# Kernel optimization log

Hardware: AMD Instinct MI355X
Metric: run time of the kernel (lower is better)

Reference implementation:

```python
import jax, jax.numpy as jnp
import numpy as np

PH = PW = 7      # aligned output bins (output_size=(aligned_width, aligned_height)=(7,7))
SR = 2           # fixed bilinear sampling ratio per bin (approximates torchvision adaptive ratio)
NUM_LEVELS = 4


def _sample_offsets(n_bins):
    # offsets (in units of bin size) of SR samples per bin: py + (iy+0.5)/SR
    k = jnp.arange(n_bins * SR, dtype=jnp.float32)
    return (k // SR) + ((k % SR) + 0.5) / SR  # [n_bins*SR]


def _bilinear_gather(feat, ys, xs):
    # feat [C,H,W]; ys [N,I]; xs [N,J] -> [N,C,I,J]  (torchvision bilinear_interpolate semantics)
    C, H, W = feat.shape
    vy = (ys >= -1.0) & (ys <= H)
    vx = (xs >= -1.0) & (xs <= W)
    y = jnp.clip(ys, 0.0, H - 1.0)
    x = jnp.clip(xs, 0.0, W - 1.0)
    y0 = jnp.floor(y)
    x0 = jnp.floor(x)
    ly = y - y0
    lx = x - x0
    y0i = y0.astype(jnp.int32)
    x0i = x0.astype(jnp.int32)
    y1i = jnp.minimum(y0i + 1, H - 1)
    x1i = jnp.minimum(x0i + 1, W - 1)

    def g(yi, xi):
        return feat[:, yi[:, :, None], xi[:, None, :]]  # [C,N,I,J]

    w00 = (1.0 - ly)[:, :, None] * (1.0 - lx)[:, None, :]
    w01 = (1.0 - ly)[:, :, None] * lx[:, None, :]
    w10 = ly[:, :, None] * (1.0 - lx)[:, None, :]
    w11 = ly[:, :, None] * lx[:, None, :]
    val = (w00 * g(y0i, x0i) + w01 * g(y0i, x1i)
           + w10 * g(y1i, x0i) + w11 * g(y1i, x1i))  # [C,N,I,J]
    mask = vy[:, :, None] & vx[:, None, :]            # [N,I,J]
    return jnp.where(mask[None], val, 0.0).transpose(1, 0, 2, 3)


def _roi_align_level(feat, boxes):
    # feat [C,H,W], boxes [N,4] xyxy in this level's coords -> [N,C,PH,PW]
    x1, y1, x2, y2 = boxes[:, 0], boxes[:, 1], boxes[:, 2], boxes[:, 3]
    rw = jnp.maximum(x2 - x1, 1.0)
    rh = jnp.maximum(y2 - y1, 1.0)
    bw = rw / PW
    bh = rh / PH
    ys = y1[:, None] + _sample_offsets(PH)[None, :] * bh[:, None]  # [N, PH*SR]
    xs = x1[:, None] + _sample_offsets(PW)[None, :] * bw[:, None]  # [N, PW*SR]
    v = _bilinear_gather(feat, ys, xs)                             # [N,C,PH*SR,PW*SR]
    N, C = v.shape[0], v.shape[1]
    return v.reshape(N, C, PH, SR, PW, SR).mean(axis=(3, 5))       # avg over samples per bin


def setup_inputs() -> dict:
    key = jax.random.key(0)
    kf0, kf1, kf2, kf3, kxy, klev = jax.random.split(key, 6)
    B, C, H0, N = 2, 256, 160, 512
    feats = {}
    for name, k, hw in (("feat0", kf0, 160), ("feat1", kf1, 80), ("feat2", kf2, 40), ("feat3", kf3, 20)):
        feats[name] = jax.random.normal(k, (B, C, hw, hw), dtype=jnp.float32)
    # boxes xyxy in base (pre-scale) coords, in [0, ~19.5]
    xy = jnp.sort(jax.random.uniform(kxy, (B, N, 2, 2), dtype=jnp.float32) * 19.0, axis=2)
    x1y1 = xy[:, :, 0, :]
    x2y2 = xy[:, :, 1, :] + 0.5  # min box size
    # level ids sorted per batch so torch's group-by-level concat order == roi index order
    levels = jnp.sort(jax.random.randint(klev, (B, N), 0, NUM_LEVELS), axis=1).astype(jnp.float32)
    z = jnp.zeros((B, N, 1), dtype=jnp.float32)
    rois = jnp.concatenate(
        [z, x1y1[..., 0:1], x1y1[..., 1:2], x2y2[..., 0:1], x2y2[..., 1:2], z, levels[..., None]], axis=-1)
    feats["rois"] = rois
    return feats


def reference(feat0, feat1, feat2, feat3, rois):
    feats = [feat0, feat1, feat2, feat3]
    B, _, H0, W0 = feat0.shape
    boxes = rois[..., 1:5]   # [B,N,4]
    levels = rois[..., 6]    # [B,N]
    pooled = 0.0
    for l, feat in enumerate(feats):
        H, W = feat.shape[2], feat.shape[3]
        sw = 8.0 * W / W0
        sh = 8.0 * H / H0
        scale = jnp.array([sw, sh, sw, sh], dtype=boxes.dtype)
        pl = jax.vmap(_roi_align_level)(feat, boxes * scale)        # [B,N,C,PH,PW]
        sel = (levels == l).astype(pl.dtype)[..., None, None, None]
        pooled = pooled + sel * pl
    # F.avg_pool2d(kernel_size=2, stride=1): 7x7 -> 6x6
    p = (pooled[..., :-1, :-1] + pooled[..., 1:, :-1]
         + pooled[..., :-1, 1:] + pooled[..., 1:, 1:]) * 0.25
    B_, N_, C, h, w = p.shape
    return p.reshape(B_ * N_, C * h * w)
```

## Files before the change

### kernel.cpp

```cpp
#include <hip/hip_runtime.h>
#include <hip/hip_bf16.h>
#include <hip/hip_fp16.h>


#define PH 7
#define C_CH 256
#define N_ROI 512
#define H0 160

#define P0 25600
#define P1 6400
#define P2 1600
#define P3 400
#define OFF0 0ull
#define OFF1 (OFF0 + 2ull * C_CH * P0)
#define OFF2 (OFF1 + 2ull * C_CH * P1)
#define OFF3 (OFF2 + 2ull * C_CH * P2)
#define WS_HALFS (OFF3 + 2ull * C_CH * P3)

#define NB0 (400 * 8)
#define NB1 (100 * 8)
#define NB2 (25 * 8)
#define NB3 (7 * 8)
#define NB_ALL (NB0 + NB1 + NB2 + NB3)

__global__ __launch_bounds__(256) void transpose_f16_kernel(
    const float* __restrict__ f0, const float* __restrict__ f1,
    const float* __restrict__ f2, const float* __restrict__ f3,
    __half* __restrict__ ws)
{
    __shared__ float tile[64 * 65];
    int bid = blockIdx.x;
    const float* in; __half* outp; int P;
    if (bid < NB0)                  {              in = f0; outp = ws + OFF0; P = P0; }
    else if (bid < NB0 + NB1)       { bid -= NB0;  in = f1; outp = ws + OFF1; P = P1; }
    else if (bid < NB0 + NB1 + NB2) { bid -= NB0 + NB1; in = f2; outp = ws + OFF2; P = P2; }
    else                            { bid -= NB0 + NB1 + NB2; in = f3; outp = ws + OFF3; P = P3; }
    const int tiles_p = (P + 63) >> 6;
    const int tp   = bid % tiles_p;
    const int rest = bid / tiles_p;
    const int c0 = (rest & 3) << 6;
    const int b  = rest >> 2;
    const int p0 = tp << 6;
    const int pmax = P - p0;

    const int t = threadIdx.x;
    const int pc  = (t & 15) << 2;
    const int cc0 = t >> 4;
    const float* A = in + ((size_t)b * C_CH + c0 + cc0) * (size_t)P + p0 + pc;
    if (pc < pmax) {
        #pragma unroll
        for (int k = 0; k < 4; ++k) {
            const float4 v = *(const float4*)(A + (size_t)(16 * k) * P);
            float* dst = tile + (cc0 + 16 * k) * 65 + pc;
            dst[0] = v.x; dst[1] = v.y; dst[2] = v.z; dst[3] = v.w;
        }
    }
    __syncthreads();
    const int c2  = t & 31;
    const int pr0 = t >> 5;
    __half2* O = (__half2*)outp + ((size_t)b * P + p0) * (C_CH / 2) + (c0 >> 1) + c2;
    #pragma unroll
    for (int k = 0; k < 8; ++k) {
        const int pp = pr0 + 8 * k;
        if (pp < pmax) {
            const float fx = tile[(2 * c2)     * 65 + pp];
            const float fy = tile[(2 * c2 + 1) * 65 + pp];
            O[(size_t)pp * (C_CH / 2)] = __floats2half2_rn(fx, fy);
        }
    }
}

__global__ __launch_bounds__(256) void roialign_kernel(
    const __half* __restrict__ ws,
    const float* __restrict__ rois, float* __restrict__ out)
{
    const int roi = blockIdx.x;
    const int b   = roi / N_ROI;
    const float* r = rois + (size_t)roi * 7;

    __shared__ int    s_y0[14], s_y1[14], s_x0[14], s_x1[14];
    __shared__ float  s_ly[14], s_lx[14], s_vy[14], s_vx[14];
    __shared__ float4 s_w[14][14];
    __shared__ float2 s_out2[128 * 36];

    const int lev = (int)r[6];
    int H; const __half* ft;
    if      (lev == 0) { H = 160; ft = ws + OFF0; }
    else if (lev == 1) { H = 80;  ft = ws + OFF1; }
    else if (lev == 2) { H = 40;  ft = ws + OFF2; }
    else               { H = 20;  ft = ws + OFF3; }
    const int W = H;
    const int P = H * W;

    const float scale = (8.0f * (float)H) / (float)H0;
    const float x1 = r[1] * scale, y1 = r[2] * scale;
    const float x2 = r[3] * scale, y2 = r[4] * scale;
    const float bw = fmaxf(x2 - x1, 1.0f) * (1.0f / (float)PH);
    const float bh = fmaxf(y2 - y1, 1.0f) * (1.0f / (float)PH);

    const int t = threadIdx.x;
    if (t < 14) {
        const float off = (float)(t >> 1) + 0.25f + 0.5f * (float)(t & 1);
        const float ys  = y1 + off * bh;
        s_vy[t] = (ys >= -1.0f && ys <= (float)H) ? 1.0f : 0.0f;
        const float y  = fminf(fmaxf(ys, 0.0f), (float)(H - 1));
        const float yf = floorf(y);
        s_ly[t] = y - yf;
        const int y0 = (int)yf;
        s_y0[t] = y0 * (W * (C_CH / 2));
        s_y1[t] = min(y0 + 1, H - 1) * (W * (C_CH / 2));
    } else if (t < 28) {
        const int k = t - 14;
        const float off = (float)(k >> 1) + 0.25f + 0.5f * (float)(k & 1);
        const float xs  = x1 + off * bw;
        s_vx[k] = (xs >= -1.0f && xs <= (float)W) ? 1.0f : 0.0f;
        const float x  = fminf(fmaxf(xs, 0.0f), (float)(W - 1));
        const float xf = floorf(x);
        s_lx[k] = x - xf;
        const int x0 = (int)xf;
        s_x0[k] = x0 * (C_CH / 2);
        s_x1[k] = min(x0 + 1, W - 1) * (C_CH / 2);
    }
    __syncthreads();

    if (t < 196) {
        const int sy = t / 14, sx = t - 14 * sy;
        const float ly = s_ly[sy], lx = s_lx[sx];
        const float v  = 0.25f * s_vy[sy] * s_vx[sx];
        const float hy = v * ly;
        const float my = v - hy;
        s_w[sy][sx] = make_float4(my - my * lx, my * lx, hy - hy * lx, hy * lx);
    }
    __syncthreads();

    const int g  = t >> 7;
    const int c2 = t & 127;
    const __half2* __restrict__ cbase =
        (const __half2*)ft + (size_t)b * P * (C_CH / 2) + c2;

    const int i0 = g ? 3 : 0;
    float prevx[7], prevy[7];
    float2* __restrict__ sOut = s_out2 + c2 * 36;

    for (int i = i0; i < i0 + 4; ++i) {
        float curx[7], cury[7];
        #pragma unroll
        for (int j = 0; j < 7; ++j) { curx[j] = 0.0f; cury[j] = 0.0f; }

        #pragma unroll
        for (int syk = 0; syk < 2; ++syk) {
            const int sy = 2 * i + syk;
            const __half2* __restrict__ q0 = cbase + s_y0[sy];
            const __half2* __restrict__ q1 = cbase + s_y1[sy];
            #pragma unroll
            for (int j = 0; j < 7; ++j) {
                #pragma unroll
                for (int sxk = 0; sxk < 2; ++sxk) {
                    const int sx = 2 * j + sxk;
                    const float4 w = s_w[sy][sx];
                    const int xa = s_x0[sx], xb = s_x1[sx];
                    const __half2 h00 = q0[xa], h01 = q0[xb];
                    const __half2 h10 = q1[xa], h11 = q1[xb];
                    curx[j] += w.x * __low2float(h00)  + w.y * __low2float(h01)
                             + w.z * __low2float(h10)  + w.w * __low2float(h11);
                    cury[j] += w.x * __high2float(h00) + w.y * __high2float(h01)
                             + w.z * __high2float(h10) + w.w * __high2float(h11);
                }
            }
        }

        if (i > i0) {
            const int row = i - 1;
            #pragma unroll
            for (int j = 0; j < 6; ++j) {
                sOut[row * 6 + j] = make_float2(
                    0.25f * (prevx[j] + prevx[j + 1] + curx[j] + curx[j + 1]),
                    0.25f * (prevy[j] + prevy[j + 1] + cury[j] + cury[j + 1]));
            }
        }
        #pragma unroll
        for (int j = 0; j < 7; ++j) { prevx[j] = curx[j]; prevy[j] = cury[j]; }
    }

    __syncthreads();
    const float* __restrict__ sflat = (const float*)s_out2;
    float* __restrict__ orow = out + (size_t)roi * (C_CH * 36);
    #pragma unroll
    for (int e = t; e < C_CH * 36; e += 256) {
        const int cc = e / 36;
        const int kk = e - 36 * cc;
        orow[e] = sflat[(cc >> 1) * 72 + 2 * kk + (cc & 1)];
    }
}

__global__ __launch_bounds__(256) void roialign_direct_kernel(
    const float* __restrict__ f0, const float* __restrict__ f1,
    const float* __restrict__ f2, const float* __restrict__ f3,
    const float* __restrict__ rois, float* __restrict__ out)
{
    const int roi = blockIdx.x;
    const int b   = roi / N_ROI;
    const float* r = rois + (size_t)roi * 7;

    __shared__ int   s_y0[14], s_y1[14], s_x0[14], s_x1[14];
    __shared__ float s_ly[14], s_lx[14], s_vy[14], s_vx[14];

    const int lev = (int)r[6];
    int H; const float* f;
    if      (lev == 0) { H = 160; f = f0; }
    else if (lev == 1) { H = 80;  f = f1; }
    else if (lev == 2) { H = 40;  f = f2; }
    else               { H = 20;  f = f3; }
    const int W = H;
    const float scale = (8.0f * (float)H) / (float)H0;
    const float x1 = r[1] * scale, y1 = r[2] * scale;
    const float x2 = r[3] * scale, y2 = r[4] * scale;
    const float bw = fmaxf(x2 - x1, 1.0f) * (1.0f / (float)PH);
    const float bh = fmaxf(y2 - y1, 1.0f) * (1.0f / (float)PH);

    const int t = threadIdx.x;
    if (t < 14) {
        const float off = (float)(t >> 1) + 0.25f + 0.5f * (float)(t & 1);
        const float ys  = y1 + off * bh;
        s_vy[t] = (ys >= -1.0f && ys <= (float)H) ? 1.0f : 0.0f;
        const float y  = fminf(fmaxf(ys, 0.0f), (float)(H - 1));
        const float yf = floorf(y);
        s_ly[t] = y - yf;
        const int y0 = (int)yf;
        s_y0[t] = y0 * W;
        s_y1[t] = min(y0 + 1, H - 1) * W;
    } else if (t < 28) {
        const int k = t - 14;
        const float off = (float)(k >> 1) + 0.25f + 0.5f * (float)(k & 1);
        const float xs  = x1 + off * bw;
        s_vx[k] = (xs >= -1.0f && xs <= (float)W) ? 1.0f : 0.0f;
        const float x  = fminf(fmaxf(xs, 0.0f), (float)(W - 1));
        const float xf = floorf(x);
        s_lx[k] = x - xf;
        const int x0 = (int)xf;
        s_x0[k] = x0;
        s_x1[k] = min(x0 + 1, W - 1);
    }
    __syncthreads();

    const int c = t;
    const float* __restrict__ fc = f + ((size_t)b * C_CH + c) * (size_t)(H * W);
    float* __restrict__ o_base = out + (size_t)roi * (C_CH * 36) + (size_t)c * 36;
    float prev[PH];

    for (int i = 0; i < PH; ++i) {
        const int   sy0 = 2 * i, sy1 = 2 * i + 1;
        const float lya = s_ly[sy0], vya = s_vy[sy0];
        const float lyb = s_ly[sy1], vyb = s_vy[sy1];
        const float* ra0 = fc + s_y0[sy0];
        const float* ra1 = fc + s_y1[sy0];
        const float* rb0 = fc + s_y0[sy1];
        const float* rb1 = fc + s_y1[sy1];
        float cur[PH];
        #pragma unroll
        for (int j = 0; j < PH; ++j) {
            float acc = 0.0f;
            #pragma unroll
            for (int sj = 0; sj < 2; ++sj) {
                const int   sx = 2 * j + sj;
                const int   x0 = s_x0[sx], x1i = s_x1[sx];
                const float lx = s_lx[sx], vx = s_vx[sx];
                {
                    const float f00 = ra0[x0], f01 = ra0[x1i];
                    const float f10 = ra1[x0], f11 = ra1[x1i];
                    const float top = f00 + lx * (f01 - f00);
                    const float bot = f10 + lx * (f11 - f10);
                    acc += (vya * vx) * (top + lya * (bot - top));
                }
                {
                    const float f00 = rb0[x0], f01 = rb0[x1i];
                    const float f10 = rb1[x0], f11 = rb1[x1i];
                    const float top = f00 + lx * (f01 - f00);
                    const float bot = f10 + lx * (f11 - f10);
                    acc += (vyb * vx) * (top + lyb * (bot - top));
                }
            }
            cur[j] = acc * 0.25f;
        }
        if (i > 0) {
            float* o = o_base + (size_t)(i - 1) * 6;
            #pragma unroll
            for (int j = 0; j < 6; ++j)
                o[j] = 0.25f * (prev[j] + prev[j + 1] + cur[j] + cur[j + 1]);
        }
        #pragma unroll
        for (int j = 0; j < PH; ++j) prev[j] = cur[j];
    }
}

extern "C" void kernel_launch(void* const* d_in, const int* in_sizes, int n_in,
                              void* d_out, int out_size, void* d_ws, size_t ws_size,
                              hipStream_t stream) {
    const float* f0   = (const float*)d_in[0];
    const float* f1   = (const float*)d_in[1];
    const float* f2   = (const float*)d_in[2];
    const float* f3   = (const float*)d_in[3];
    const float* rois = (const float*)d_in[4];
    float* out = (float*)d_out;

    const int n_rois = in_sizes[4] / 7;
    const size_t need = WS_HALFS * sizeof(__half);

    if (d_ws != nullptr && ws_size >= need) {
        __half* ws = (__half*)d_ws;
        transpose_f16_kernel<<<NB_ALL, 256, 0, stream>>>(f0, f1, f2, f3, ws);
        roialign_kernel<<<n_rois, 256, 0, stream>>>(ws, rois, out);
    } else {
        roialign_direct_kernel<<<n_rois, 256, 0, stream>>>(f0, f1, f2, f3, rois, out);
    }
}
```

Before: 148.3 us.

## Use scalar offsets, half-precision LDS staging and occupancy hint in roialign kernel

```diff
diff --git a/kernel.cpp b/kernel.cpp
--- a/kernel.cpp
+++ b/kernel.cpp
@@ -23,6 +23,10 @@
 #define NB2 (25 * 8)
 #define NB3 (7 * 8)
 #define NB_ALL (NB0 + NB1 + NB2 + NB3)
+
+__device__ __forceinline__ int rfl_i(int x) {
+    return __builtin_amdgcn_readfirstlane(x);
+}
 
 __global__ __launch_bounds__(256) void transpose_f16_kernel(
     const float* __restrict__ f0, const float* __restrict__ f1,
@@ -71,7 +75,7 @@
     }
 }
 
-__global__ __launch_bounds__(256) void roialign_kernel(
+__global__ __launch_bounds__(256, 6) void roialign_kernel(
     const __half* __restrict__ ws,
     const float* __restrict__ rois, float* __restrict__ out)
 {
@@ -82,7 +86,7 @@
     __shared__ int    s_y0[14], s_y1[14], s_x0[14], s_x1[14];
     __shared__ float  s_ly[14], s_lx[14], s_vy[14], s_vx[14];
     __shared__ float4 s_w[14][14];
-    __shared__ float2 s_out2[128 * 36];
+    __shared__ __half2 s_hout[128 * 37];
 
     const int lev = (int)r[6];
     int H; const __half* ft;
@@ -136,14 +140,22 @@
 
     const int g  = t >> 7;
     const int c2 = t & 127;
-    const __half2* __restrict__ cbase =
-        (const __half2*)ft + (size_t)b * P * (C_CH / 2) + c2;
+    const __half2* __restrict__ tb =
+        (const __half2*)ft + (size_t)b * P * (C_CH / 2);
+
+    int xoA[14], xoB[14];
+    #pragma unroll
+    for (int s = 0; s < 14; ++s) {
+        xoA[s] = rfl_i(s_x0[s]);
+        xoB[s] = rfl_i(s_x1[s]);
+    }
 
     const int i0 = g ? 3 : 0;
     float prevx[7], prevy[7];
-    float2* __restrict__ sOut = s_out2 + c2 * 36;
-
-    for (int i = i0; i < i0 + 4; ++i) {
+    __half2* __restrict__ sOut = s_hout + c2 * 37;
+
+    for (int ii = 0; ii < 4; ++ii) {
+        const int i = i0 + ii;
         float curx[7], cury[7];
         #pragma unroll
         for (int j = 0; j < 7; ++j) { curx[j] = 0.0f; cury[j] = 0.0f; }
@@ -151,17 +163,20 @@
         #pragma unroll
         for (int syk = 0; syk < 2; ++syk) {
             const int sy = 2 * i + syk;
-            const __half2* __restrict__ q0 = cbase + s_y0[sy];
-            const __half2* __restrict__ q1 = cbase + s_y1[sy];
+            const int yo0 = rfl_i(s_y0[sy]);
+            const int yo1 = rfl_i(s_y1[sy]);
+            const __half2* __restrict__ r0 = tb + yo0;
+            const __half2* __restrict__ r1 = tb + yo1;
             #pragma unroll
             for (int j = 0; j < 7; ++j) {
                 #pragma unroll
                 for (int sxk = 0; sxk < 2; ++sxk) {
                     const int sx = 2 * j + sxk;
                     const float4 w = s_w[sy][sx];
-                    const int xa = s_x0[sx], xb = s_x1[sx];
-                    const __half2 h00 = q0[xa], h01 = q0[xb];
-                    const __half2 h10 = q1[xa], h11 = q1[xb];
+                    const __half2 h00 = (r0 + xoA[sx])[c2];
+                    const __half2 h01 = (r0 + xoB[sx])[c2];
+                    const __half2 h10 = (r1 + xoA[sx])[c2];
+                    const __half2 h11 = (r1 + xoB[sx])[c2];
                     curx[j] += w.x * __low2float(h00)  + w.y * __low2float(h01)
                              + w.z * __low2float(h10)  + w.w * __low2float(h11);
                     cury[j] += w.x * __high2float(h00) + w.y * __high2float(h01)
@@ -170,11 +185,11 @@
             }
         }
 
-        if (i > i0) {
+        if (ii > 0) {
             const int row = i - 1;
             #pragma unroll
             for (int j = 0; j < 6; ++j) {
-                sOut[row * 6 + j] = make_float2(
+                sOut[row * 6 + j] = __floats2half2_rn(
                     0.25f * (prevx[j] + prevx[j + 1] + curx[j] + curx[j + 1]),
                     0.25f * (prevy[j] + prevy[j + 1] + cury[j] + cury[j + 1]));
             }
@@ -184,13 +199,13 @@
     }
 
     __syncthreads();
-    const float* __restrict__ sflat = (const float*)s_out2;
     float* __restrict__ orow = out + (size_t)roi * (C_CH * 36);
     #pragma unroll
     for (int e = t; e < C_CH * 36; e += 256) {
         const int cc = e / 36;
         const int kk = e - 36 * cc;
-        orow[e] = sflat[(cc >> 1) * 72 + 2 * kk + (cc & 1)];
+        const __half2 v = s_hout[(cc >> 1) * 37 + kk];
+        orow[e] = (cc & 1) ? __high2float(v) : __low2float(v);
     }
 }
 
```

New measurement: 167.8 us. 1.13x slower.
